# Performance work log

Measured on AMD Instinct MI355X. Metric: run time of the kernel, lower is better.

The kernel has to match this reference:

```python
import jax, jax.numpy as jnp
import numpy as np

N_NODES = 50000
N_EDGES = 800000
IN_F = 128
OUT_F = 64


def setup_inputs() -> dict:
    key = jax.random.key(0)
    k1, k2, k3, k4, k5 = jax.random.split(key, 5)
    x = jax.random.normal(k1, (N_NODES, IN_F), dtype=jnp.float32)
    edge_index = jax.random.randint(k2, (2, N_EDGES), 0, N_NODES, dtype=jnp.int64)
    edge_weight = jax.random.uniform(k3, (N_EDGES,), dtype=jnp.float32)
    # Linear(in,out,bias=False): store as [in, out] so h = x @ W
    W = jax.random.normal(k4, (IN_F, OUT_F), dtype=jnp.float32) * (1.0 / np.sqrt(IN_F))
    # Linear(2*out, 1, bias=False): store as [2*out] vector
    a = jax.random.normal(k5, (2 * OUT_F,), dtype=jnp.float32) * (1.0 / np.sqrt(2 * OUT_F))
    return {"x": x, "edge_index": edge_index, "edge_weight": edge_weight, "W": W, "a": a}


def reference(x, edge_index, edge_weight, W, a):
    N = x.shape[0]
    F = W.shape[1]
    src, dst = edge_index[0], edge_index[1]
    h = x @ W  # [N, F]
    # a([h_src ; h_dst]) == h_src @ a[:F] + h_dst @ a[F:]  (no edge-level concat)
    s_src = h @ a[:F]   # [N]
    s_dst = h @ a[F:]   # [N]
    e = s_src[src] + s_dst[dst]            # [E]
    alpha = jax.nn.leaky_relu(e, negative_slope=0.2) * edge_weight
    alpha = alpha - jnp.max(alpha)         # global max subtraction, as in source
    alpha_exp = jnp.exp(alpha)             # [E]
    alpha_sum = jax.ops.segment_sum(alpha_exp, dst, num_segments=N)  # [N]
    alpha_norm = alpha_exp / (alpha_sum[dst] + 1e-8)                 # [E] (dropout = identity, eval mode)
    out = jax.ops.segment_sum(h[src] * alpha_norm[:, None], dst, num_segments=N)  # [N, F]
    return jax.nn.elu(out)
```

## Files before the change

### kernel.cpp

```cpp
#include <hip/hip_runtime.h>
#include <hip/hip_bf16.h>
#include <math.h>

#define FIN 128
#define FOUT 64
#define TM 64
#define XS_STRIDE 136

#define DB 64
#define CAP 1280
#define NBMAX 1024
#define TILE_A 4096
#define EPT_A 16

typedef __attribute__((ext_vector_type(8))) short short8;
typedef __attribute__((ext_vector_type(4))) float floatx4;

static __device__ __forceinline__ unsigned short f2bf(float f) {
  __hip_bfloat16 b = __float2bfloat16(f);
  return *reinterpret_cast<unsigned short*>(&b);
}

__global__ __launch_bounds__(256) void k_gemm(
    const float* __restrict__ x, const float* __restrict__ W,
    const float* __restrict__ a, unsigned short* __restrict__ hbf,
    float* __restrict__ s_src, float* __restrict__ s_dst,
    int* __restrict__ bcur, int N)
{
  __shared__ unsigned short xsb[TM][XS_STRIDE];
  __shared__ unsigned short Wl[FOUT][XS_STRIDE];
  int t = threadIdx.x;
  int n0 = blockIdx.x * TM;

  int gid = blockIdx.x * 256 + t;
  if (gid < 800) bcur[gid] = 0;

  for (int i = t; i < FIN * FOUT; i += 256) {
    int k = i >> 6, f = i & 63;
    Wl[f][k] = f2bf(W[i]);
  }

#pragma unroll
  for (int i = 0; i < 8; i++) {
    int idx = t + i * 256;
    int row = idx >> 5, c4 = (idx & 31) * 4;
    int n = n0 + row;
    float4 v = make_float4(0.f, 0.f, 0.f, 0.f);
    if (n < N) v = *(const float4*)&x[(size_t)n * FIN + c4];
    ushort4 u = make_ushort4(f2bf(v.x), f2bf(v.y), f2bf(v.z), f2bf(v.w));
    *(ushort4*)&xsb[row][c4] = u;
  }
  __syncthreads();

  int lane = t & 63, w = t >> 6;
  int m = lane & 15, q = lane >> 4;

  short8 bf[4][4];
#pragma unroll
  for (int k0 = 0; k0 < 4; k0++)
#pragma unroll
    for (int j = 0; j < 4; j++)
      bf[k0][j] = *(const short8*)&Wl[j * 16 + m][k0 * 32 + q * 8];

  floatx4 acc[4];
#pragma unroll
  for (int j = 0; j < 4; j++) acc[j] = (floatx4){0.f, 0.f, 0.f, 0.f};

#pragma unroll
  for (int k0 = 0; k0 < 4; k0++) {
    short8 af = *(const short8*)&xsb[w * 16 + m][k0 * 32 + q * 8];
#pragma unroll
    for (int j = 0; j < 4; j++)
      acc[j] = __builtin_amdgcn_mfma_f32_16x16x32_bf16(af, bf[k0][j], acc[j], 0, 0, 0);
  }

  float av1[4], av2[4];
#pragma unroll
  for (int j = 0; j < 4; j++) {
    av1[j] = a[j * 16 + m];
    av2[j] = a[FOUT + j * 16 + m];
  }
  float s1r[4], s2r[4];
#pragma unroll
  for (int r = 0; r < 4; r++) {
    float c1 = 0.f, c2 = 0.f;
#pragma unroll
    for (int j = 0; j < 4; j++) {
      c1 = fmaf(acc[j][r], av1[j], c1);
      c2 = fmaf(acc[j][r], av2[j], c2);
    }
    s1r[r] = c1; s2r[r] = c2;
  }
#pragma unroll
  for (int o = 1; o < 16; o <<= 1) {
#pragma unroll
    for (int r = 0; r < 4; r++) {
      s1r[r] += __shfl_xor(s1r[r], o);
      s2r[r] += __shfl_xor(s2r[r], o);
    }
  }

#pragma unroll
  for (int j = 0; j < 4; j++)
#pragma unroll
    for (int r = 0; r < 4; r++) {
      int n = n0 + w * 16 + q * 4 + r;
      if (n < N) hbf[(size_t)n * FOUT + j * 16 + m] = f2bf(acc[j][r]);
    }
  if (m == 0) {
#pragma unroll
    for (int r = 0; r < 4; r++) {
      int n = n0 + w * 16 + q * 4 + r;
      if (n < N) { s_src[n] = s1r[r]; s_dst[n] = s2r[r]; }
    }
  }
}

__global__ __launch_bounds__(256) void k_bucketA(
    const int* __restrict__ src, const int* __restrict__ dst,
    const float* __restrict__ ew, const float* __restrict__ s_src,
    const float* __restrict__ s_dst, int* __restrict__ bcur,
    uint2* __restrict__ inter, int E, int nbuck)
{
  __shared__ uint2 stage[TILE_A];
  __shared__ int hist[NBMAX];
  __shared__ int sbase[NBMAX];
  __shared__ int gbase[NBMAX];
  __shared__ int wsum[4];

  int t = threadIdx.x;
  int base = blockIdx.x * TILE_A;
  int cntTile = E - base; if (cntTile > TILE_A) cntTile = TILE_A;

  for (int i = t; i < nbuck; i += 256) hist[i] = 0;
  __syncthreads();

  unsigned key[EPT_A]; float aev[EPT_A]; int lpos[EPT_A];
#pragma unroll
  for (int i = 0; i < EPT_A; i++) {
    int e = base + t + i * 256;
    lpos[i] = -1;
    if (e < E) {
      int s = src[e], d = dst[e];
      float v = s_src[s] + s_dst[d];
      v = (v > 0.f) ? v : 0.2f * v;
      v *= ew[e];
      key[i] = ((unsigned)d << 16) | (unsigned)s;
      aev[i] = __expf(v);
      lpos[i] = atomicAdd(&hist[d >> 6], 1);
    }
  }
  __syncthreads();

  int i0 = t * 4;
  int c0 = (i0 + 0 < nbuck) ? hist[i0 + 0] : 0;
  int c1 = (i0 + 1 < nbuck) ? hist[i0 + 1] : 0;
  int c2 = (i0 + 2 < nbuck) ? hist[i0 + 2] : 0;
  int c3 = (i0 + 3 < nbuck) ? hist[i0 + 3] : 0;
  int ts = c0 + c1 + c2 + c3;
  int lane = t & 63, wid = t >> 6;
  int inc = ts;
#pragma unroll
  for (int o = 1; o < 64; o <<= 1) {
    int up = __shfl_up(inc, o);
    if (lane >= o) inc += up;
  }
  if (lane == 63) wsum[wid] = inc;
  __syncthreads();
  int woff = 0;
  for (int w = 0; w < wid; w++) woff += wsum[w];
  int run = woff + inc - ts;
  if (i0 + 0 < nbuck) sbase[i0 + 0] = run; run += c0;
  if (i0 + 1 < nbuck) sbase[i0 + 1] = run; run += c1;
  if (i0 + 2 < nbuck) sbase[i0 + 2] = run; run += c2;
  if (i0 + 3 < nbuck) sbase[i0 + 3] = run;
  __syncthreads();

  for (int b = t; b < nbuck; b += 256)
    if (hist[b] > 0) gbase[b] = atomicAdd(&bcur[b], hist[b]);
  __syncthreads();

#pragma unroll
  for (int i = 0; i < EPT_A; i++)
    if (lpos[i] >= 0) {
      int b = key[i] >> 22;
      stage[sbase[b] + lpos[i]] = make_uint2(key[i], __float_as_uint(aev[i]));
    }
  __syncthreads();

  for (int i = t; i < cntTile; i += 256) {
    uint2 en = stage[i];
    int b = en.x >> 22;
    int slot = gbase[b] + (i - sbase[b]);
    if (slot < CAP) inter[(size_t)b * CAP + slot] = en;
  }
}

__global__ __launch_bounds__(512) void k_bucketB(
    const uint2* __restrict__ inter, const int* __restrict__ bcur,
    const unsigned short* __restrict__ hbf, float* __restrict__ out, int N)
{
  __shared__ uint2 ss[CAP];
  __shared__ int hist[DB];
  __shared__ int rp[DB];
  int b = blockIdx.x;
  int t = threadIdx.x;
  int cnt = bcur[b]; if (cnt > CAP) cnt = CAP;

  if (t < DB) hist[t] = 0;
  __syncthreads();

  const uint2* bin = inter + (size_t)b * CAP;
  unsigned kx[3], ka[3]; int lp[3], dl[3];
#pragma unroll
  for (int i = 0; i < 3; i++) {
    int p = t + i * 512;
    lp[i] = -1;
    if (p < cnt) {
      uint2 en = bin[p];
      kx[i] = en.x; ka[i] = en.y;
      dl[i] = (en.x >> 16) & (DB - 1);
      lp[i] = atomicAdd(&hist[dl[i]], 1);
    }
  }
  __syncthreads();

  if (t < DB) {
    int v = hist[t];
    int inc = v;
#pragma unroll
    for (int o = 1; o < 64; o <<= 1) {
      int up = __shfl_up(inc, o);
      if (t >= o) inc += up;
    }
    rp[t] = inc - v;
  }
  __syncthreads();

#pragma unroll
  for (int i = 0; i < 3; i++)
    if (lp[i] >= 0) ss[rp[dl[i]] + lp[i]] = make_uint2(kx[i], ka[i]);
  __syncthreads();

  int grp = t >> 3, l = t & 7;
  int n = b * DB + grp;
  int beg = rp[grp];
  int end = beg + hist[grp];

  float acc[8];
#pragma unroll
  for (int i = 0; i < 8; i++) acc[i] = 0.f;
  float asum = 0.f;

  for (int p = beg; p < end; p += 4) {
    float aev[4]; uint4 rv[4];
#pragma unroll
    for (int u = 0; u < 4; u++) {
      aev[u] = 0.f;
      rv[u] = make_uint4(0u, 0u, 0u, 0u);
      if (p + u < end) {
        uint2 e = ss[p + u];
        aev[u] = __uint_as_float(e.y);
        rv[u] = ((const uint4*)(hbf + ((size_t)(e.x & 0xFFFFu) << 6)))[l];
      }
    }
#pragma unroll
    for (int u = 0; u < 4; u++) {
      asum += aev[u];
      const unsigned* uu = (const unsigned*)&rv[u];
#pragma unroll
      for (int i = 0; i < 4; i++) {
        float2 f = __bfloat1622float2(*(const __hip_bfloat162*)&uu[i]);
        acc[2 * i]     = fmaf(aev[u], f.x, acc[2 * i]);
        acc[2 * i + 1] = fmaf(aev[u], f.y, acc[2 * i + 1]);
      }
    }
  }

  if (n < N) {
    float inv = 1.f / (asum + 1e-8f);
    float v[8];
#pragma unroll
    for (int i = 0; i < 8; i++) {
      v[i] = acc[i] * inv;
      v[i] = (v[i] > 0.f) ? v[i] : expm1f(v[i]);
    }
    float* op = &out[(size_t)n * FOUT + l * 8];
    *(float4*)op       = make_float4(v[0], v[1], v[2], v[3]);
    *(float4*)(op + 4) = make_float4(v[4], v[5], v[6], v[7]);
  }
}

extern "C" void kernel_launch(void* const* d_in, const int* in_sizes, int n_in,
                              void* d_out, int out_size, void* d_ws, size_t ws_size,
                              hipStream_t stream)
{
  const float* x  = (const float*)d_in[0];
  const int*   ei = (const int*)d_in[1];
  const float* ew = (const float*)d_in[2];
  const float* W  = (const float*)d_in[3];
  const float* a  = (const float*)d_in[4];
  float* out = (float*)d_out;

  const int N = in_sizes[0] / FIN;
  const int E = in_sizes[2];
  const int* src = ei;
  const int* dst = ei + E;
  const int nbuck = (N + DB - 1) / DB;

  unsigned short* hbf = (unsigned short*)d_ws;
  float* ssrc  = (float*)(hbf + (size_t)N * FOUT);
  float* sdst  = ssrc + N;
  int*   bcur  = (int*)(sdst + N);
  uint2* inter = (uint2*)(bcur + 800);

  k_gemm<<<(N + TM - 1) / TM, 256, 0, stream>>>(x, W, a, hbf, ssrc, sdst, bcur, N);
  k_bucketA<<<(E + TILE_A - 1) / TILE_A, 256, 0, stream>>>(src, dst, ew, ssrc, sdst, bcur, inter, E, nbuck);
  k_bucketB<<<nbuck, 512, 0, stream>>>(inter, bcur, hbf, out, N);
}
```

Baseline: 128.7 us.

## Fuse three kernels into one persistent kernel with software grid barriers

Replaces the three launches (GEMM, edge bucketing, per-bucket aggregation) with a single persistent kernel of 512 blocks that loops over tiles. Phases are separated by atomic-counter grid barriers. The goal is to remove launch gaps and inter-kernel drain. A hipMemsetAsync is added, plus an occupancy query on every call to guard against deadlock. The bucket and aggregation phases now run with 256 threads instead of 512, and the edge tile shrinks to 2048. This lowers per-block parallelism, and the barrier spinning adds latency.

```diff
diff --git a/kernel.cpp b/kernel.cpp
--- a/kernel.cpp
+++ b/kernel.cpp
@@ -9,9 +9,16 @@
 
 #define DB 64
 #define CAP 1280
-#define NBMAX 1024
+#define NT 256
+#define FGRID 512
+
+#define TAF 2048
+#define EAF 8
+#define NBF 800
+
 #define TILE_A 4096
 #define EPT_A 16
+#define NBMAX 1024
 
 typedef __attribute__((ext_vector_type(8))) short short8;
 typedef __attribute__((ext_vector_type(4))) float floatx4;
@@ -20,6 +27,303 @@
   __hip_bfloat16 b = __float2bfloat16(f);
   return *reinterpret_cast<unsigned short*>(&b);
 }
+
+static __device__ __forceinline__ void acc8(const uint4& r, float ae, float* acc) {
+  const unsigned* u = (const unsigned*)&r;
+#pragma unroll
+  for (int i = 0; i < 4; i++) {
+    float2 f = __bfloat1622float2(*(const __hip_bfloat162*)&u[i]);
+    acc[2 * i]     = fmaf(ae, f.x, acc[2 * i]);
+    acc[2 * i + 1] = fmaf(ae, f.y, acc[2 * i + 1]);
+  }
+}
+
+static __device__ __forceinline__ void grid_barrier(int* cnt, int* flag, int nb) {
+  __syncthreads();
+  if (threadIdx.x == 0) {
+    __threadfence();
+    int prev = __hip_atomic_fetch_add(cnt, 1, __ATOMIC_ACQ_REL, __HIP_MEMORY_SCOPE_AGENT);
+    if (prev == nb - 1) {
+      __hip_atomic_store(flag, 1, __ATOMIC_RELEASE, __HIP_MEMORY_SCOPE_AGENT);
+    } else {
+      while (__hip_atomic_load(flag, __ATOMIC_ACQUIRE, __HIP_MEMORY_SCOPE_AGENT) == 0)
+        __builtin_amdgcn_s_sleep(8);
+    }
+    __threadfence();
+  }
+  __syncthreads();
+}
+
+
+struct SG { unsigned short xsb[TM][XS_STRIDE]; unsigned short Wl[FOUT][XS_STRIDE]; };
+struct SA { uint2 stage[TAF]; int hist[NBF]; int sbase[NBF]; int gbase[NBF]; int wsum[4]; };
+struct SB { uint2 ss[CAP]; int hist[DB]; int rp[DB]; };
+union SMem { SG g; SA a; SB b; };
+
+__global__ __launch_bounds__(NT, 2) void k_fusedsw(
+    const float* __restrict__ x, const float* __restrict__ W,
+    const float* __restrict__ a, const int* __restrict__ src,
+    const int* __restrict__ dst, const float* __restrict__ ew,
+    unsigned short* __restrict__ hbf, float* __restrict__ s_src,
+    float* __restrict__ s_dst, int* __restrict__ bcur,
+    uint2* __restrict__ inter, float* __restrict__ out,
+    int* __restrict__ bar, int N, int E, int nbuck)
+{
+  __shared__ SMem sm;
+  int t = threadIdx.x;
+  int nb = gridDim.x;
+
+  for (int i = blockIdx.x * NT + t; i < 800; i += nb * NT) bcur[i] = 0;
+
+  int ntileG = (N + TM - 1) / TM;
+  for (int tile = blockIdx.x; tile < ntileG; tile += nb) {
+    int n0 = tile * TM;
+
+    for (int i = t; i < FIN * FOUT; i += NT) {
+      int k = i >> 6, f = i & 63;
+      sm.g.Wl[f][k] = f2bf(W[i]);
+    }
+
+#pragma unroll
+    for (int i = 0; i < 8; i++) {
+      int idx = t + i * NT;
+      int row = idx >> 5, c4 = (idx & 31) * 4;
+      int n = n0 + row;
+      float4 v = make_float4(0.f, 0.f, 0.f, 0.f);
+      if (n < N) v = *(const float4*)&x[(size_t)n * FIN + c4];
+      ushort4 u = make_ushort4(f2bf(v.x), f2bf(v.y), f2bf(v.z), f2bf(v.w));
+      *(ushort4*)&sm.g.xsb[row][c4] = u;
+    }
+    __syncthreads();
+
+    int lane = t & 63, w = t >> 6;
+    int m = lane & 15, q = lane >> 4;
+
+    short8 bf[4][4];
+#pragma unroll
+    for (int k0 = 0; k0 < 4; k0++)
+#pragma unroll
+      for (int j = 0; j < 4; j++)
+        bf[k0][j] = *(const short8*)&sm.g.Wl[j * 16 + m][k0 * 32 + q * 8];
+
+    floatx4 acc[4];
+#pragma unroll
+    for (int j = 0; j < 4; j++) acc[j] = (floatx4){0.f, 0.f, 0.f, 0.f};
+
+#pragma unroll
+    for (int k0 = 0; k0 < 4; k0++) {
+      short8 af = *(const short8*)&sm.g.xsb[w * 16 + m][k0 * 32 + q * 8];
+#pragma unroll
+      for (int j = 0; j < 4; j++)
+        acc[j] = __builtin_amdgcn_mfma_f32_16x16x32_bf16(af, bf[k0][j], acc[j], 0, 0, 0);
+    }
+
+    float av1[4], av2[4];
+#pragma unroll
+    for (int j = 0; j < 4; j++) {
+      av1[j] = a[j * 16 + m];
+      av2[j] = a[FOUT + j * 16 + m];
+    }
+    float s1r[4], s2r[4];
+#pragma unroll
+    for (int r = 0; r < 4; r++) {
+      float c1 = 0.f, c2 = 0.f;
+#pragma unroll
+      for (int j = 0; j < 4; j++) {
+        c1 = fmaf(acc[j][r], av1[j], c1);
+        c2 = fmaf(acc[j][r], av2[j], c2);
+      }
+      s1r[r] = c1; s2r[r] = c2;
+    }
+#pragma unroll
+    for (int o = 1; o < 16; o <<= 1) {
+#pragma unroll
+      for (int r = 0; r < 4; r++) {
+        s1r[r] += __shfl_xor(s1r[r], o);
+        s2r[r] += __shfl_xor(s2r[r], o);
+      }
+    }
+
+#pragma unroll
+    for (int j = 0; j < 4; j++)
+#pragma unroll
+      for (int r = 0; r < 4; r++) {
+        int n = n0 + w * 16 + q * 4 + r;
+        if (n < N) hbf[(size_t)n * FOUT + j * 16 + m] = f2bf(acc[j][r]);
+      }
+    if (m == 0) {
+#pragma unroll
+      for (int r = 0; r < 4; r++) {
+        int n = n0 + w * 16 + q * 4 + r;
+        if (n < N) { s_src[n] = s1r[r]; s_dst[n] = s2r[r]; }
+      }
+    }
+    __syncthreads();
+  }
+
+  grid_barrier(&bar[0], &bar[1], nb);
+
+  int ntileA = (E + TAF - 1) / TAF;
+  for (int tile = blockIdx.x; tile < ntileA; tile += nb) {
+    int base = tile * TAF;
+    int cntTile = E - base; if (cntTile > TAF) cntTile = TAF;
+
+    for (int i = t; i < nbuck; i += NT) sm.a.hist[i] = 0;
+    __syncthreads();
+
+    unsigned key[EAF]; float aev[EAF]; int lpos[EAF];
+#pragma unroll
+    for (int i = 0; i < EAF; i++) {
+      int e = base + t + i * NT;
+      lpos[i] = -1;
+      if (e < E) {
+        int s = src[e], d = dst[e];
+        float v = s_src[s] + s_dst[d];
+        v = (v > 0.f) ? v : 0.2f * v;
+        v *= ew[e];
+        key[i] = ((unsigned)d << 16) | (unsigned)s;
+        aev[i] = __expf(v);
+        lpos[i] = atomicAdd(&sm.a.hist[d >> 6], 1);
+      }
+    }
+    __syncthreads();
+
+    int i0 = t * 4;
+    int c0 = (i0 + 0 < nbuck) ? sm.a.hist[i0 + 0] : 0;
+    int c1 = (i0 + 1 < nbuck) ? sm.a.hist[i0 + 1] : 0;
+    int c2 = (i0 + 2 < nbuck) ? sm.a.hist[i0 + 2] : 0;
+    int c3 = (i0 + 3 < nbuck) ? sm.a.hist[i0 + 3] : 0;
+    int ts = c0 + c1 + c2 + c3;
+    int lane = t & 63, wid = t >> 6;
+    int inc = ts;
+#pragma unroll
+    for (int o = 1; o < 64; o <<= 1) {
+      int up = __shfl_up(inc, o);
+      if (lane >= o) inc += up;
+    }
+    if (lane == 63) sm.a.wsum[wid] = inc;
+    __syncthreads();
+    int woff = 0;
+    for (int w = 0; w < wid; w++) woff += sm.a.wsum[w];
+    int run = woff + inc - ts;
+    if (i0 + 0 < nbuck) sm.a.sbase[i0 + 0] = run; run += c0;
+    if (i0 + 1 < nbuck) sm.a.sbase[i0 + 1] = run; run += c1;
+    if (i0 + 2 < nbuck) sm.a.sbase[i0 + 2] = run; run += c2;
+    if (i0 + 3 < nbuck) sm.a.sbase[i0 + 3] = run;
+    __syncthreads();
+
+    for (int b = t; b < nbuck; b += NT)
+      if (sm.a.hist[b] > 0) sm.a.gbase[b] = atomicAdd(&bcur[b], sm.a.hist[b]);
+    __syncthreads();
+
+#pragma unroll
+    for (int i = 0; i < EAF; i++)
+      if (lpos[i] >= 0) {
+        int b = key[i] >> 22;
+        sm.a.stage[sm.a.sbase[b] + lpos[i]] = make_uint2(key[i], __float_as_uint(aev[i]));
+      }
+    __syncthreads();
+
+    for (int i = t; i < cntTile; i += NT) {
+      uint2 en = sm.a.stage[i];
+      int b = en.x >> 22;
+      int slot = sm.a.gbase[b] + (i - sm.a.sbase[b]);
+      if (slot < CAP) inter[(size_t)b * CAP + slot] = en;
+    }
+    __syncthreads();
+  }
+
+  grid_barrier(&bar[2], &bar[3], nb);
+
+  for (int b = blockIdx.x; b < nbuck; b += nb) {
+    int cnt = bcur[b]; if (cnt > CAP) cnt = CAP;
+
+    if (t < DB) sm.b.hist[t] = 0;
+    __syncthreads();
+
+    const uint2* bin = inter + (size_t)b * CAP;
+    unsigned kx[5], ka[5]; int lp[5], dl[5];
+#pragma unroll
+    for (int i = 0; i < 5; i++) {
+      int p = t + i * NT;
+      lp[i] = -1;
+      if (p < cnt) {
+        uint2 en = bin[p];
+        kx[i] = en.x; ka[i] = en.y;
+        dl[i] = (en.x >> 16) & (DB - 1);
+        lp[i] = atomicAdd(&sm.b.hist[dl[i]], 1);
+      }
+    }
+    __syncthreads();
+
+    if (t < DB) {
+      int v = sm.b.hist[t];
+      int inc = v;
+#pragma unroll
+      for (int o = 1; o < 64; o <<= 1) {
+        int up = __shfl_up(inc, o);
+        if (t >= o) inc += up;
+      }
+      sm.b.rp[t] = inc - v;
+    }
+    __syncthreads();
+
+#pragma unroll
+    for (int i = 0; i < 5; i++)
+      if (lp[i] >= 0) sm.b.ss[sm.b.rp[dl[i]] + lp[i]] = make_uint2(kx[i], ka[i]);
+    __syncthreads();
+
+    int grp = t >> 2, l = t & 3;
+    int n = b * DB + grp;
+    int beg = sm.b.rp[grp];
+    int end = beg + sm.b.hist[grp];
+
+    float acc[16];
+#pragma unroll
+    for (int i = 0; i < 16; i++) acc[i] = 0.f;
+    float asum = 0.f;
+
+    for (int p = beg; p < end; p += 4) {
+      float aev[4]; uint4 ra[4], rb[4];
+#pragma unroll
+      for (int u = 0; u < 4; u++) {
+        aev[u] = 0.f;
+        ra[u] = make_uint4(0u, 0u, 0u, 0u);
+        rb[u] = make_uint4(0u, 0u, 0u, 0u);
+        if (p + u < end) {
+          uint2 e = sm.b.ss[p + u];
+          aev[u] = __uint_as_float(e.y);
+          const uint4* r = (const uint4*)(hbf + ((size_t)(e.x & 0xFFFFu) << 6));
+          ra[u] = r[2 * l];
+          rb[u] = r[2 * l + 1];
+        }
+      }
+#pragma unroll
+      for (int u = 0; u < 4; u++) {
+        asum += aev[u];
+        acc8(ra[u], aev[u], acc);
+        acc8(rb[u], aev[u], acc + 8);
+      }
+    }
+
+    if (n < N) {
+      float inv = 1.f / (asum + 1e-8f);
+      float* op = &out[(size_t)n * FOUT + l * 16];
+#pragma unroll
+      for (int c = 0; c < 4; c++) {
+        float v0 = acc[c * 4 + 0] * inv, v1 = acc[c * 4 + 1] * inv;
+        float v2 = acc[c * 4 + 2] * inv, v3 = acc[c * 4 + 3] * inv;
+        v0 = (v0 > 0.f) ? v0 : expm1f(v0);
+        v1 = (v1 > 0.f) ? v1 : expm1f(v1);
+        v2 = (v2 > 0.f) ? v2 : expm1f(v2);
+        v3 = (v3 > 0.f) ? v3 : expm1f(v3);
+        *(float4*)(op + c * 4) = make_float4(v0, v1, v2, v3);
+      }
+    }
+    __syncthreads();
+  }
+}
+
 
 __global__ __launch_bounds__(256) void k_gemm(
     const float* __restrict__ x, const float* __restrict__ W,
@@ -313,8 +617,18 @@
   float* sdst  = ssrc + N;
   int*   bcur  = (int*)(sdst + N);
   uint2* inter = (uint2*)(bcur + 800);
-
-  k_gemm<<<(N + TM - 1) / TM, 256, 0, stream>>>(x, W, a, hbf, ssrc, sdst, bcur, N);
-  k_bucketA<<<(E + TILE_A - 1) / TILE_A, 256, 0, stream>>>(src, dst, ew, ssrc, sdst, bcur, inter, E, nbuck);
-  k_bucketB<<<nbuck, 512, 0, stream>>>(inter, bcur, hbf, out, N);
-}
+  int*   bar   = (int*)(inter + (size_t)nbuck * CAP);
+
+  int occ = 0;
+  hipError_t qerr = hipOccupancyMaxActiveBlocksPerMultiprocessor(&occ, k_fusedsw, NT, 0);
+
+  if (qerr == hipSuccess && occ >= 2) {
+    hipMemsetAsync(bar, 0, 4 * sizeof(int), stream);
+    k_fusedsw<<<FGRID, NT, 0, stream>>>(x, W, a, src, dst, ew, hbf, ssrc, sdst,
+                                        bcur, inter, out, bar, N, E, nbuck);
+  } else {
+    k_gemm<<<(N + TM - 1) / TM, 256, 0, stream>>>(x, W, a, hbf, ssrc, sdst, bcur, N);
+    k_bucketA<<<(E + TILE_A - 1) / TILE_A, 256, 0, stream>>>(src, dst, ew, ssrc, sdst, bcur, inter, E, nbuck);
+    k_bucketB<<<nbuck, 512, 0, stream>>>(inter, bcur, hbf, out, N);
+  }
+}
```

Measured after the change: 373.2 us. +189.9%, slower.

## Replace two-level bucket sort with per-destination atomic scatter slots

Applied to the files above, without the earlier changes.

Drops the tiled bucket histogram and in-shared-memory reordering. Each edge now takes its slot with a global atomic on a per-node counter and is written into a fixed-capacity per-destination array, which the gather kernel reads directly. This removes the LDS staging, prefix scans and extra sort pass, at the cost of many scattered global atomics and writes. Edges beyond 128 per node are silently dropped.

```diff
diff --git a/kernel.cpp b/kernel.cpp
--- a/kernel.cpp
+++ b/kernel.cpp
@@ -7,11 +7,8 @@
 #define TM 64
 #define XS_STRIDE 136
 
-#define DB 64
-#define CAP 1280
-#define NBMAX 1024
-#define TILE_A 4096
-#define EPT_A 16
+#define CAP_D 128
+#define EPT_S 2
 
 typedef __attribute__((ext_vector_type(8))) short short8;
 typedef __attribute__((ext_vector_type(4))) float floatx4;
@@ -25,7 +22,7 @@
     const float* __restrict__ x, const float* __restrict__ W,
     const float* __restrict__ a, unsigned short* __restrict__ hbf,
     float* __restrict__ s_src, float* __restrict__ s_dst,
-    int* __restrict__ bcur, int N)
+    int* __restrict__ dcur, int N)
 {
   __shared__ unsigned short xsb[TM][XS_STRIDE];
   __shared__ unsigned short Wl[FOUT][XS_STRIDE];
@@ -33,7 +30,7 @@
   int n0 = blockIdx.x * TM;
 
   int gid = blockIdx.x * 256 + t;
-  if (gid < 800) bcur[gid] = 0;
+  if (gid < N) dcur[gid] = 0;
 
   for (int i = t; i < FIN * FOUT; i += 256) {
     int k = i >> 6, f = i & 63;
@@ -116,152 +113,69 @@
   }
 }
 
-__global__ __launch_bounds__(256) void k_bucketA(
+__global__ __launch_bounds__(256) void k_scatter(
     const int* __restrict__ src, const int* __restrict__ dst,
     const float* __restrict__ ew, const float* __restrict__ s_src,
-    const float* __restrict__ s_dst, int* __restrict__ bcur,
-    uint2* __restrict__ inter, int E, int nbuck)
-{
-  __shared__ uint2 stage[TILE_A];
-  __shared__ int hist[NBMAX];
-  __shared__ int sbase[NBMAX];
-  __shared__ int gbase[NBMAX];
-  __shared__ int wsum[4];
-
+    const float* __restrict__ s_dst, int* __restrict__ dcur,
+    uint2* __restrict__ inter, int E)
+{
   int t = threadIdx.x;
-  int base = blockIdx.x * TILE_A;
-  int cntTile = E - base; if (cntTile > TILE_A) cntTile = TILE_A;
-
-  for (int i = t; i < nbuck; i += 256) hist[i] = 0;
-  __syncthreads();
-
-  unsigned key[EPT_A]; float aev[EPT_A]; int lpos[EPT_A];
-#pragma unroll
-  for (int i = 0; i < EPT_A; i++) {
+  int base = blockIdx.x * (256 * EPT_S);
+
+  int sv[EPT_S], dv[EPT_S]; float evw[EPT_S]; int ok[EPT_S];
+#pragma unroll
+  for (int i = 0; i < EPT_S; i++) {
     int e = base + t + i * 256;
-    lpos[i] = -1;
-    if (e < E) {
-      int s = src[e], d = dst[e];
-      float v = s_src[s] + s_dst[d];
+    ok[i] = (e < E);
+    if (ok[i]) { sv[i] = src[e]; dv[i] = dst[e]; evw[i] = ew[e]; }
+  }
+  float ae[EPT_S];
+#pragma unroll
+  for (int i = 0; i < EPT_S; i++) {
+    if (ok[i]) {
+      float v = s_src[sv[i]] + s_dst[dv[i]];
       v = (v > 0.f) ? v : 0.2f * v;
-      v *= ew[e];
-      key[i] = ((unsigned)d << 16) | (unsigned)s;
-      aev[i] = __expf(v);
-      lpos[i] = atomicAdd(&hist[d >> 6], 1);
-    }
-  }
-  __syncthreads();
-
-  int i0 = t * 4;
-  int c0 = (i0 + 0 < nbuck) ? hist[i0 + 0] : 0;
-  int c1 = (i0 + 1 < nbuck) ? hist[i0 + 1] : 0;
-  int c2 = (i0 + 2 < nbuck) ? hist[i0 + 2] : 0;
-  int c3 = (i0 + 3 < nbuck) ? hist[i0 + 3] : 0;
-  int ts = c0 + c1 + c2 + c3;
-  int lane = t & 63, wid = t >> 6;
-  int inc = ts;
-#pragma unroll
-  for (int o = 1; o < 64; o <<= 1) {
-    int up = __shfl_up(inc, o);
-    if (lane >= o) inc += up;
-  }
-  if (lane == 63) wsum[wid] = inc;
-  __syncthreads();
-  int woff = 0;
-  for (int w = 0; w < wid; w++) woff += wsum[w];
-  int run = woff + inc - ts;
-  if (i0 + 0 < nbuck) sbase[i0 + 0] = run; run += c0;
-  if (i0 + 1 < nbuck) sbase[i0 + 1] = run; run += c1;
-  if (i0 + 2 < nbuck) sbase[i0 + 2] = run; run += c2;
-  if (i0 + 3 < nbuck) sbase[i0 + 3] = run;
-  __syncthreads();
-
-  for (int b = t; b < nbuck; b += 256)
-    if (hist[b] > 0) gbase[b] = atomicAdd(&bcur[b], hist[b]);
-  __syncthreads();
-
-#pragma unroll
-  for (int i = 0; i < EPT_A; i++)
-    if (lpos[i] >= 0) {
-      int b = key[i] >> 22;
-      stage[sbase[b] + lpos[i]] = make_uint2(key[i], __float_as_uint(aev[i]));
-    }
-  __syncthreads();
-
-  for (int i = t; i < cntTile; i += 256) {
-    uint2 en = stage[i];
-    int b = en.x >> 22;
-    int slot = gbase[b] + (i - sbase[b]);
-    if (slot < CAP) inter[(size_t)b * CAP + slot] = en;
-  }
-}
-
-__global__ __launch_bounds__(512) void k_bucketB(
-    const uint2* __restrict__ inter, const int* __restrict__ bcur,
+      v *= evw[i];
+      ae[i] = __expf(v);
+    }
+  }
+#pragma unroll
+  for (int i = 0; i < EPT_S; i++) {
+    if (ok[i]) {
+      int slot = atomicAdd(&dcur[dv[i]], 1);
+      if (slot < CAP_D)
+        inter[(size_t)dv[i] * CAP_D + slot] = make_uint2((unsigned)sv[i], __float_as_uint(ae[i]));
+    }
+  }
+}
+
+__global__ __launch_bounds__(512) void k_gather(
+    const uint2* __restrict__ inter, const int* __restrict__ dcur,
     const unsigned short* __restrict__ hbf, float* __restrict__ out, int N)
 {
-  __shared__ uint2 ss[CAP];
-  __shared__ int hist[DB];
-  __shared__ int rp[DB];
-  int b = blockIdx.x;
   int t = threadIdx.x;
-  int cnt = bcur[b]; if (cnt > CAP) cnt = CAP;
-
-  if (t < DB) hist[t] = 0;
-  __syncthreads();
-
-  const uint2* bin = inter + (size_t)b * CAP;
-  unsigned kx[3], ka[3]; int lp[3], dl[3];
-#pragma unroll
-  for (int i = 0; i < 3; i++) {
-    int p = t + i * 512;
-    lp[i] = -1;
-    if (p < cnt) {
-      uint2 en = bin[p];
-      kx[i] = en.x; ka[i] = en.y;
-      dl[i] = (en.x >> 16) & (DB - 1);
-      lp[i] = atomicAdd(&hist[dl[i]], 1);
-    }
-  }
-  __syncthreads();
-
-  if (t < DB) {
-    int v = hist[t];
-    int inc = v;
-#pragma unroll
-    for (int o = 1; o < 64; o <<= 1) {
-      int up = __shfl_up(inc, o);
-      if (t >= o) inc += up;
-    }
-    rp[t] = inc - v;
-  }
-  __syncthreads();
-
-#pragma unroll
-  for (int i = 0; i < 3; i++)
-    if (lp[i] >= 0) ss[rp[dl[i]] + lp[i]] = make_uint2(kx[i], ka[i]);
-  __syncthreads();
-
   int grp = t >> 3, l = t & 7;
-  int n = b * DB + grp;
-  int beg = rp[grp];
-  int end = beg + hist[grp];
+  int n = blockIdx.x * 64 + grp;
+  if (n >= N) return;
+
+  int cnt = dcur[n]; if (cnt > CAP_D) cnt = CAP_D;
+  const uint2* run = inter + (size_t)n * CAP_D;
 
   float acc[8];
 #pragma unroll
   for (int i = 0; i < 8; i++) acc[i] = 0.f;
   float asum = 0.f;
 
-  for (int p = beg; p < end; p += 4) {
+  for (int p = 0; p < cnt; p += 4) {
     float aev[4]; uint4 rv[4];
 #pragma unroll
     for (int u = 0; u < 4; u++) {
       aev[u] = 0.f;
       rv[u] = make_uint4(0u, 0u, 0u, 0u);
-      if (p + u < end) {
-        uint2 e = ss[p + u];
+      if (p + u < cnt) {
+        uint2 e = run[p + u];
         aev[u] = __uint_as_float(e.y);
-        rv[u] = ((const uint4*)(hbf + ((size_t)(e.x & 0xFFFFu) << 6)))[l];
+        rv[u] = ((const uint4*)(hbf + ((size_t)e.x << 6)))[l];
       }
     }
 #pragma unroll
@@ -277,18 +191,16 @@
     }
   }
 
-  if (n < N) {
-    float inv = 1.f / (asum + 1e-8f);
-    float v[8];
-#pragma unroll
-    for (int i = 0; i < 8; i++) {
-      v[i] = acc[i] * inv;
-      v[i] = (v[i] > 0.f) ? v[i] : expm1f(v[i]);
-    }
-    float* op = &out[(size_t)n * FOUT + l * 8];
-    *(float4*)op       = make_float4(v[0], v[1], v[2], v[3]);
-    *(float4*)(op + 4) = make_float4(v[4], v[5], v[6], v[7]);
-  }
+  float inv = 1.f / (asum + 1e-8f);
+  float v[8];
+#pragma unroll
+  for (int i = 0; i < 8; i++) {
+    v[i] = acc[i] * inv;
+    v[i] = (v[i] > 0.f) ? v[i] : expm1f(v[i]);
+  }
+  float* op = &out[(size_t)n * FOUT + l * 8];
+  *(float4*)op       = make_float4(v[0], v[1], v[2], v[3]);
+  *(float4*)(op + 4) = make_float4(v[4], v[5], v[6], v[7]);
 }
 
 extern "C" void kernel_launch(void* const* d_in, const int* in_sizes, int n_in,
@@ -306,15 +218,14 @@
   const int E = in_sizes[2];
   const int* src = ei;
   const int* dst = ei + E;
-  const int nbuck = (N + DB - 1) / DB;
 
   unsigned short* hbf = (unsigned short*)d_ws;
   float* ssrc  = (float*)(hbf + (size_t)N * FOUT);
   float* sdst  = ssrc + N;
-  int*   bcur  = (int*)(sdst + N);
-  uint2* inter = (uint2*)(bcur + 800);
-
-  k_gemm<<<(N + TM - 1) / TM, 256, 0, stream>>>(x, W, a, hbf, ssrc, sdst, bcur, N);
-  k_bucketA<<<(E + TILE_A - 1) / TILE_A, 256, 0, stream>>>(src, dst, ew, ssrc, sdst, bcur, inter, E, nbuck);
-  k_bucketB<<<nbuck, 512, 0, stream>>>(inter, bcur, hbf, out, N);
-}
+  int*   dcur  = (int*)(sdst + N);
+  uint2* inter = (uint2*)(dcur + N);
+
+  k_gemm<<<(N + TM - 1) / TM, 256, 0, stream>>>(x, W, a, hbf, ssrc, sdst, dcur, N);
+  k_scatter<<<(E + 256 * EPT_S - 1) / (256 * EPT_S), 256, 0, stream>>>(src, dst, ew, ssrc, sdst, dcur, inter, E);
+  k_gather<<<(N + 63) / 64, 512, 0, stream>>>(inter, dcur, hbf, out, N);
+}
```

Measured after the change: 155.3 us. +20.6%, slower.
